# Kernel optimization log

Measured on AMD Instinct MI355X. Metric: run time of the kernel, lower is better.

The kernel has to match this reference:

```python
import jax, jax.numpy as jnp
import numpy as np

N_EMBD = 384
NUM_HEADS = 6
HEAD_SIZE = 64


def setup_inputs() -> dict:
    key = jax.random.key(0)
    k1, k2, k3, k4 = jax.random.split(key, 4)
    B, T = 32, 1024
    x = jax.random.normal(k1, (B, T, N_EMBD), dtype=jnp.float32)
    # torch Linear(n_embd, 3*n_embd, bias=False): store as [in, out]
    s_attn = 1.0 / np.sqrt(N_EMBD)
    W_attn = jax.random.uniform(k2, (N_EMBD, 3 * N_EMBD), dtype=jnp.float32, minval=-s_attn, maxval=s_attn)
    W_proj = jax.random.uniform(k3, (N_EMBD, N_EMBD), dtype=jnp.float32, minval=-s_attn, maxval=s_attn)
    b_proj = jax.random.uniform(k4, (N_EMBD,), dtype=jnp.float32, minval=-s_attn, maxval=s_attn)
    return {"x": x, "W_attn": W_attn, "W_proj": W_proj, "b_proj": b_proj}


def reference(x, W_attn, W_proj, b_proj):
    B, T, C = x.shape
    H, D = NUM_HEADS, HEAD_SIZE
    qkv = x @ W_attn                      # [B, T, 3C]
    q, k, v = jnp.split(qkv, 3, axis=2)   # each [B, T, C]
    # [B, H, T, D]
    q = q.reshape(B, T, H, D).transpose(0, 2, 1, 3)
    k = k.reshape(B, T, H, D).transpose(0, 2, 1, 3)
    v = v.reshape(B, T, H, D).transpose(0, 2, 1, 3)
    scale = 1.0 / jnp.sqrt(jnp.asarray(D, dtype=x.dtype))
    scores = jnp.einsum("bhqd,bhkd->bhqk", q, k) * scale  # [B, H, T, T]
    causal = jnp.tril(jnp.ones((T, T), dtype=bool))
    scores = jnp.where(causal, scores, jnp.asarray(-jnp.inf, dtype=scores.dtype))
    attn = jax.nn.softmax(scores, axis=-1)
    y = jnp.einsum("bhqk,bhkd->bhqd", attn, v)             # [B, H, T, D]
    y = y.transpose(0, 2, 1, 3).reshape(B, T, C)
    # dropout is inactive in eval mode
    return y @ W_proj + b_proj
```

## Files before the change

kernel.cpp:

```cpp
#include <hip/hip_runtime.h>
#include <hip/hip_bf16.h>

#define DEV __device__ __forceinline__

typedef __attribute__((ext_vector_type(4))) float f32x4;
typedef __bf16 bf16x8 __attribute__((ext_vector_type(8)));

static DEV unsigned short f2bf(float f) {
    union { float f; unsigned u; } x; x.f = f;
    unsigned r = x.u + 0x7fffu + ((x.u >> 16) & 1u);
    return (unsigned short)(r >> 16);
}

static DEV f32x4 zero4() { f32x4 v; v[0] = 0.f; v[1] = 0.f; v[2] = 0.f; v[3] = 0.f; return v; }

#define GL1(p) ((const __attribute__((address_space(1))) void*)(p))
#define LDS3(p) ((__attribute__((address_space(3))) void*)(p))


__global__ __launch_bounds__(256) void k_prep(
    const float* __restrict__ x, unsigned short* __restrict__ xb,
    const float* __restrict__ Wa, unsigned short* __restrict__ WaT,
    const float* __restrict__ Wp, unsigned short* __restrict__ WpT)
{
    int i = blockIdx.x * 256 + threadIdx.x;
    if (i < 3145728) {
        float4 v = reinterpret_cast<const float4*>(x)[i];
        ushort4 o;
        o.x = f2bf(v.x); o.y = f2bf(v.y); o.z = f2bf(v.z); o.w = f2bf(v.w);
        reinterpret_cast<ushort4*>(xb)[i] = o;
    } else if (i < 3145728 + 442368) {
        int j = i - 3145728;
        int n = j / 384, k = j - n * 384;
        WaT[j] = f2bf(Wa[(size_t)k * 1152 + n]);
    } else if (i < 3145728 + 442368 + 147456) {
        int j = i - (3145728 + 442368);
        int n = j / 384, k = j - n * 384;
        WpT[j] = f2bf(Wp[(size_t)k * 384 + n]);
    }
}


template <int SWAP>
static DEV void gemm_mainloop(
    const unsigned short* __restrict__ A,
    const unsigned short* __restrict__ B,
    int m0, int n0, int tid,
    f32x4 (&acc)[4][4],
    unsigned short (&lA)[128][64], unsigned short (&lB)[128][64])
{
    const int K = 384;
    const int w = tid >> 6, lane = tid & 63;
    const int wm = (w >> 1) * 64, wn = (w & 1) * 64;
    const int lr = lane & 15, lg = lane >> 4;
    const int lrow = lane >> 3;
    const int lcol = ((lane & 7) ^ lrow) * 8;

    for (int kb = 0; kb < K; kb += 64) {
        __syncthreads();
#pragma unroll
        for (int c = 0; c < 4; ++c) {
            int rb = (w * 4 + c) * 8;
            __builtin_amdgcn_global_load_lds(GL1(&A[(size_t)(m0 + rb + lrow) * K + kb + lcol]),
                                             LDS3(&lA[rb][0]), 16, 0, 0);
            __builtin_amdgcn_global_load_lds(GL1(&B[(size_t)(n0 + rb + lrow) * K + kb + lcol]),
                                             LDS3(&lB[rb][0]), 16, 0, 0);
        }
        __syncthreads();

        bf16x8 af[4][2], bfr[4][2];
#pragma unroll
        for (int kc = 0; kc < 2; ++kc) {
#pragma unroll
            for (int t = 0; t < 4; ++t) {
                int ga = ((kc * 4 + lg) ^ (lr & 7)) * 8;
                af[t][kc]  = *(const bf16x8*)&lA[wm + t * 16 + lr][ga];
                bfr[t][kc] = *(const bf16x8*)&lB[wn + t * 16 + lr][ga];
            }
        }
#pragma unroll
        for (int kc = 0; kc < 2; ++kc)
#pragma unroll
            for (int mt = 0; mt < 4; ++mt)
#pragma unroll
                for (int nt = 0; nt < 4; ++nt)
                    acc[mt][nt] = SWAP
                        ? __builtin_amdgcn_mfma_f32_16x16x32_bf16(bfr[nt][kc], af[mt][kc], acc[mt][nt], 0, 0, 0)
                        : __builtin_amdgcn_mfma_f32_16x16x32_bf16(af[mt][kc], bfr[nt][kc], acc[mt][nt], 0, 0, 0);
    }
}


__global__ __launch_bounds__(256) void k_gemm_qkv(
    const unsigned short* __restrict__ A,
    const unsigned short* __restrict__ B,
    unsigned short* __restrict__ Qb, unsigned short* __restrict__ Kb,
    unsigned short* __restrict__ Vb)
{
    __shared__ unsigned short lA[128][64];
    __shared__ unsigned short lB[128][64];

    const int bid = blockIdx.x;
    const int xcd = bid & 7, s = bid >> 3;
    const int mi = xcd * 32 + s / 9;
    const int cj = s % 9;
    const int m0 = mi * 128, n0 = cj * 128;

    const int tid = threadIdx.x;
    const int w = tid >> 6, lane = tid & 63;
    const int wm = (w >> 1) * 64, wn = (w & 1) * 64;
    const int lr = lane & 15, lg = lane >> 4;

    f32x4 acc[4][4];
#pragma unroll
    for (int i = 0; i < 4; i++)
#pragma unroll
        for (int j = 0; j < 4; j++) acc[i][j] = zero4();

    if (cj < 6) {
        gemm_mainloop<1>(A, B, m0, n0, tid, acc, lA, lB);
        const int which = cj / 3;
#pragma unroll
        for (int mt = 0; mt < 4; ++mt) {
            int row = m0 + wm + mt * 16 + lr;
            int bb = row >> 10, tloc = row & 1023;
#pragma unroll
            for (int nt = 0; nt < 4; ++nt) {
                int col = n0 + wn + nt * 16 + lg * 4;
                int c = col - which * 384;
                int hh = c >> 6, d0 = c & 63;
                size_t bh = (size_t)bb * 6 + hh;
                int kc = (d0 >> 5) & 1;
                int ln = (tloc & 15) + 16 * ((d0 >> 3) & 3);
                int e0 = d0 & 7;
                union { __bf16 h4[4]; uint2 u; } pk;
                if (which == 0) {
#pragma unroll
                    for (int r = 0; r < 4; ++r)
                        pk.h4[r] = (__bf16)(acc[mt][nt][r] * 0.18033688f);
                    int qt = tloc >> 5, fmt = (tloc >> 4) & 1;
                    *(uint2*)&Qb[((((bh * 32 + qt) * 2 + fmt) * 2 + kc) * 64 + ln) * 8 + e0] = pk.u;
                } else {
#pragma unroll
                    for (int r = 0; r < 4; ++r)
                        pk.h4[r] = (__bf16)acc[mt][nt][r];
                    int ktt = tloc >> 6, fnt = (tloc >> 4) & 3;
                    *(uint2*)&Kb[((((bh * 16 + ktt) * 4 + fnt) * 2 + kc) * 64 + ln) * 8 + e0] = pk.u;
                }
            }
        }
    } else {
        gemm_mainloop<0>(A, B, m0, n0, tid, acc, lA, lB);
#pragma unroll
        for (int nt = 0; nt < 4; ++nt) {
            int col = n0 + wn + nt * 16 + lr;
            int c = col - 768;
            int hh = c >> 6, d = c & 63;
            int fnt = d >> 4;
#pragma unroll
            for (int mt = 0; mt < 4; ++mt) {
                int row0 = m0 + wm + mt * 16 + lg * 4;
                int bb = row0 >> 10, t0 = row0 & 1023;
                size_t bh = (size_t)bb * 6 + hh;
                int ktt = t0 >> 6, kc = (t0 >> 5) & 1, e0 = t0 & 7;
                int ln = (d & 15) + 16 * ((t0 >> 3) & 3);
                union { __bf16 h4[4]; uint2 u; } pk;
#pragma unroll
                for (int r = 0; r < 4; ++r)
                    pk.h4[r] = (__bf16)acc[mt][nt][r];
                *(uint2*)&Vb[((((bh * 16 + ktt) * 4 + fnt) * 2 + kc) * 64 + ln) * 8 + e0] = pk.u;
            }
        }
    }
}


__global__ __launch_bounds__(256) void k_gemm_proj(
    const unsigned short* __restrict__ A,
    const unsigned short* __restrict__ B,
    const float* __restrict__ bias, float* __restrict__ Out)
{
    __shared__ unsigned short lA[128][64];
    __shared__ unsigned short lB[128][64];

    const int bid = blockIdx.x;
    const int xcd = bid & 7, s = bid >> 3;
    const int mi = xcd * 32 + s / 3;
    const int cj = s % 3;
    const int m0 = mi * 128, n0 = cj * 128;

    const int tid = threadIdx.x;
    const int w = tid >> 6, lane = tid & 63;
    const int wm = (w >> 1) * 64, wn = (w & 1) * 64;
    const int lr = lane & 15, lg = lane >> 4;

    f32x4 acc[4][4];
#pragma unroll
    for (int i = 0; i < 4; i++)
#pragma unroll
        for (int j = 0; j < 4; j++) acc[i][j] = zero4();

    gemm_mainloop<1>(A, B, m0, n0, tid, acc, lA, lB);

#pragma unroll
    for (int mt = 0; mt < 4; ++mt) {
        int row = m0 + wm + mt * 16 + lr;
#pragma unroll
        for (int nt = 0; nt < 4; ++nt) {
            int col = n0 + wn + nt * 16 + lg * 4;
            f32x4 bv = *(const f32x4*)&bias[col];
            f32x4 ov;
#pragma unroll
            for (int r = 0; r < 4; ++r) ov[r] = acc[mt][nt][r] + bv[r];
            *(f32x4*)&Out[(size_t)row * 384 + col] = ov;
        }
    }
}


template <int NTM, bool MASK>
static DEV void attn_tile(
    const unsigned short* lKt, const unsigned short* lVt, unsigned short* lPw,
    const bf16x8 (&qf)[2][2], f32x4 (&o)[2][4], float (&ls)[2],
    int kt, int qw, int lane)
{
    constexpr int KCM = NTM / 2;
    const int lr = lane & 15, lg = lane >> 4;

    bf16x8 kf[NTM][2];
#pragma unroll
    for (int nt = 0; nt < NTM; ++nt)
#pragma unroll
        for (int kc = 0; kc < 2; ++kc)
            kf[nt][kc] = *(const bf16x8*)&lKt[(nt * 2 + kc) * 512 + lane * 8];

    bf16x8 vf[4][KCM];
#pragma unroll
    for (int nt = 0; nt < 4; ++nt)
#pragma unroll
        for (int kc = 0; kc < KCM; ++kc)
            vf[nt][kc] = *(const bf16x8*)&lVt[(nt * 2 + kc) * 512 + lane * 8];

    f32x4 st[2][NTM];
#pragma unroll
    for (int mt = 0; mt < 2; ++mt)
#pragma unroll
        for (int nt = 0; nt < NTM; ++nt) st[mt][nt] = zero4();

    __builtin_amdgcn_s_setprio(1);
#pragma unroll
    for (int kc = 0; kc < 2; ++kc)
#pragma unroll
        for (int mt = 0; mt < 2; ++mt)
#pragma unroll
            for (int nt = 0; nt < NTM; ++nt)
                st[mt][nt] = __builtin_amdgcn_mfma_f32_16x16x32_bf16(kf[nt][kc], qf[mt][kc], st[mt][nt], 0, 0, 0);
    __builtin_amdgcn_s_setprio(0);

#pragma unroll
    for (int mt = 0; mt < 2; ++mt) {
#pragma unroll
        for (int nt = 0; nt < NTM; ++nt) {
            union { __bf16 hh[4]; uint2 u; } pk;
            float e[4];
#pragma unroll
            for (int r = 0; r < 4; ++r) {
                float ev = __builtin_amdgcn_exp2f(st[mt][nt][r]);
                if (MASK) {
                    int kg = kt * 64 + nt * 16 + lg * 4 + r;
                    int qg = qw + mt * 16 + lr;
                    if (kg > qg) ev = 0.f;
                }
                e[r] = ev;
                pk.hh[r] = (__bf16)ev;
            }
            ls[mt] += (e[0] + e[1]) + (e[2] + e[3]);
            int ln2 = lr + 16 * ((nt & 1) * 2 + (lg >> 1));
            *(uint2*)&lPw[(mt * 2 + (nt >> 1)) * 512 + ln2 * 8 + (lg & 1) * 4] = pk.u;
        }
    }

    bf16x8 pf[2][KCM];
#pragma unroll
    for (int mt = 0; mt < 2; ++mt)
#pragma unroll
        for (int kc = 0; kc < KCM; ++kc)
            pf[mt][kc] = *(const bf16x8*)&lPw[(mt * 2 + kc) * 512 + lane * 8];

    __builtin_amdgcn_s_setprio(1);
#pragma unroll
    for (int mt = 0; mt < 2; ++mt)
#pragma unroll
        for (int nt = 0; nt < 4; ++nt)
#pragma unroll
            for (int kc = 0; kc < KCM; ++kc)
                o[mt][nt] = __builtin_amdgcn_mfma_f32_16x16x32_bf16(vf[nt][kc], pf[mt][kc], o[mt][nt], 0, 0, 0);
    __builtin_amdgcn_s_setprio(0);
}

static DEV void attn_pass(
    int gg, int w, int lane, int b, int h, int bh,
    const unsigned short* __restrict__ Qf,
    const unsigned short* __restrict__ Kbh,
    const unsigned short* __restrict__ Vbh,
    unsigned short* __restrict__ Y,
    unsigned short (&lK)[2][4096], unsigned short (&lV)[2][4096],
    unsigned short* lPw)
{
    const int lr = lane & 15, lg = lane >> 4;
    const int qt = 4 * gg + w;
    const int qw = qt * 32;
    const int nkt = qt / 2 + 1;
    const int nsteps = 2 * gg + 2;

    bf16x8 qf[2][2];
#pragma unroll
    for (int mt = 0; mt < 2; ++mt)
#pragma unroll
        for (int kc = 0; kc < 2; ++kc)
            qf[mt][kc] = *(const bf16x8*)&Qf[((((size_t)bh * 32 + qt) * 2 + mt) * 2 + kc) * 512 + lane * 8];

    f32x4 o[2][4];
    float ls[2] = {0.f, 0.f};
#pragma unroll
    for (int mt = 0; mt < 2; ++mt)
#pragma unroll
        for (int nt = 0; nt < 4; ++nt) o[mt][nt] = zero4();

    __syncthreads();

#pragma unroll
    for (int i = 0; i < 2; ++i) {
        __builtin_amdgcn_global_load_lds(GL1(Kbh + (size_t)w * 1024 + i * 512 + lane * 8),
                                         LDS3(&lK[0][w * 1024 + i * 512]), 16, 0, 0);
        __builtin_amdgcn_global_load_lds(GL1(Vbh + (size_t)w * 1024 + i * 512 + lane * 8),
                                         LDS3(&lV[0][w * 1024 + i * 512]), 16, 0, 0);
    }

    for (int kt = 0; kt < nsteps; ++kt) {
        __syncthreads();
        if (kt + 1 < nsteps) {
            int nb = (kt + 1) & 1;
#pragma unroll
            for (int i = 0; i < 2; ++i) {
                __builtin_amdgcn_global_load_lds(GL1(Kbh + (size_t)(kt + 1) * 4096 + w * 1024 + i * 512 + lane * 8),
                                                 LDS3(&lK[nb][w * 1024 + i * 512]), 16, 0, 0);
                __builtin_amdgcn_global_load_lds(GL1(Vbh + (size_t)(kt + 1) * 4096 + w * 1024 + i * 512 + lane * 8),
                                                 LDS3(&lV[nb][w * 1024 + i * 512]), 16, 0, 0);
            }
        }
        if (kt < nkt) {
            const unsigned short* lKt = lK[kt & 1];
            const unsigned short* lVt = lV[kt & 1];
            if (kt == nkt - 1) {
                if (qt & 1) attn_tile<4, true>(lKt, lVt, lPw, qf, o, ls, kt, qw, lane);
                else        attn_tile<2, true>(lKt, lVt, lPw, qf, o, ls, kt, qw, lane);
            } else {
                attn_tile<4, false>(lKt, lVt, lPw, qf, o, ls, kt, qw, lane);
            }
        }
    }

    float inv[2];
#pragma unroll
    for (int mt = 0; mt < 2; ++mt) {
        float s = ls[mt];
        s += __shfl_xor(s, 16);
        s += __shfl_xor(s, 32);
        inv[mt] = 1.0f / s;
    }
#pragma unroll
    for (int mt = 0; mt < 2; ++mt) {
#pragma unroll
        for (int nt = 0; nt < 4; ++nt) {
            union { __bf16 h4[4]; uint2 u; } pk;
#pragma unroll
            for (int r = 0; r < 4; ++r) pk.h4[r] = (__bf16)(o[mt][nt][r] * inv[mt]);
            *(uint2*)&Y[((size_t)b * 1024 + qw + mt * 16 + lr) * 384 + h * 64 + nt * 16 + lg * 4] = pk.u;
        }
    }
}

__global__ __launch_bounds__(256, 3) void k_attn(
    const unsigned short* __restrict__ Qf,
    const unsigned short* __restrict__ Kf,
    const unsigned short* __restrict__ Vf,
    unsigned short* __restrict__ Y)
{
    __shared__ unsigned short lK[2][4096];
    __shared__ unsigned short lV[2][4096];
    __shared__ unsigned short lPf[4][2048];

    const int tid = threadIdx.x;
    const int w = tid >> 6, lane = tid & 63;
    const int bh = blockIdx.x;
    const int g = blockIdx.y;
    const int b = bh / 6, h = bh - b * 6;

    const unsigned short* Kbh = Kf + (size_t)bh * 65536;
    const unsigned short* Vbh = Vf + (size_t)bh * 65536;

    attn_pass(g,     w, lane, b, h, bh, Qf, Kbh, Vbh, Y, lK, lV, lPf[w]);
    attn_pass(7 - g, w, lane, b, h, bh, Qf, Kbh, Vbh, Y, lK, lV, lPf[w]);
}


extern "C" void kernel_launch(void* const* d_in, const int* in_sizes, int n_in,
                              void* d_out, int out_size, void* d_ws, size_t ws_size,
                              hipStream_t stream)
{
    const float* x  = (const float*)d_in[0];
    const float* Wa = (const float*)d_in[1];
    const float* Wp = (const float*)d_in[2];
    const float* bp = (const float*)d_in[3];
    float* out = (float*)d_out;

    char* ws = (char*)d_ws;
    unsigned short* xb  = (unsigned short*)(ws);
    unsigned short* WaT = (unsigned short*)(ws + 25165824);
    unsigned short* WpT = (unsigned short*)(ws + 26050560);
    unsigned short* Qb  = (unsigned short*)(ws + 26345472);
    unsigned short* Kb  = (unsigned short*)(ws + 51511296);
    unsigned short* Vtb = (unsigned short*)(ws + 76677120);

    k_prep<<<14592, 256, 0, stream>>>(x, xb, Wa, WaT, Wp, WpT);
    k_gemm_qkv<<<2304, 256, 0, stream>>>(xb, WaT, Qb, Kb, Vtb);
    k_attn<<<dim3(192, 4), 256, 0, stream>>>(Qb, Kb, Vtb, xb);
    k_gemm_proj<<<768, 256, 0, stream>>>(xb, WpT, bp, out);
}
```

Measured before the change: 122.8 us.

## Process two adjacent query tiles per wave, sharing K/V register fragments

Restructures the attention kernel so each wave owns two consecutive 32-row query tiles (A and B). K and V fragments are loaded from LDS once per key tile and reused by both query tiles, which halves LDS read traffic per MFMA. The two balanced passes per block are replaced by a single pass, with block scheduling reversed so the heaviest groups launch first. Occupancy is lowered from 3 to 2 blocks per SM in launch_bounds to make room for the extra accumulator and Q registers, which reduces latency hiding and may leave load imbalance across blocks.

```diff
diff --git a/kernel.cpp b/kernel.cpp
--- a/kernel.cpp
+++ b/kernel.cpp
@@ -219,27 +219,12 @@
 
 
 template <int NTM, bool MASK>
-static DEV void attn_tile(
-    const unsigned short* lKt, const unsigned short* lVt, unsigned short* lPw,
+static DEV void attn_qtile(
+    const bf16x8 (&kf)[4][2], const bf16x8 (&vf)[4][2],
     const bf16x8 (&qf)[2][2], f32x4 (&o)[2][4], float (&ls)[2],
-    int kt, int qw, int lane)
+    unsigned short* lPw, int kt, int qw, int lr, int lg)
 {
     constexpr int KCM = NTM / 2;
-    const int lr = lane & 15, lg = lane >> 4;
-
-    bf16x8 kf[NTM][2];
-#pragma unroll
-    for (int nt = 0; nt < NTM; ++nt)
-#pragma unroll
-        for (int kc = 0; kc < 2; ++kc)
-            kf[nt][kc] = *(const bf16x8*)&lKt[(nt * 2 + kc) * 512 + lane * 8];
-
-    bf16x8 vf[4][KCM];
-#pragma unroll
-    for (int nt = 0; nt < 4; ++nt)
-#pragma unroll
-        for (int kc = 0; kc < KCM; ++kc)
-            vf[nt][kc] = *(const bf16x8*)&lVt[(nt * 2 + kc) * 512 + lane * 8];
 
     f32x4 st[2][NTM];
 #pragma unroll
@@ -285,7 +270,7 @@
     for (int mt = 0; mt < 2; ++mt)
 #pragma unroll
         for (int kc = 0; kc < KCM; ++kc)
-            pf[mt][kc] = *(const bf16x8*)&lPw[(mt * 2 + kc) * 512 + lane * 8];
+            pf[mt][kc] = *(const bf16x8*)&lPw[(mt * 2 + kc) * 512 + (lr + 16 * lg) * 8];
 
     __builtin_amdgcn_s_setprio(1);
 #pragma unroll
@@ -298,36 +283,70 @@
     __builtin_amdgcn_s_setprio(0);
 }
 
-static DEV void attn_pass(
-    int gg, int w, int lane, int b, int h, int bh,
+static DEV void attn_out(const f32x4 (&o)[2][4], const float (&ls)[2],
+                         int qw, int b, int h, int lr, int lg,
+                         unsigned short* __restrict__ Y)
+{
+    float inv[2];
+#pragma unroll
+    for (int mt = 0; mt < 2; ++mt) {
+        float s = ls[mt];
+        s += __shfl_xor(s, 16);
+        s += __shfl_xor(s, 32);
+        inv[mt] = 1.0f / s;
+    }
+#pragma unroll
+    for (int mt = 0; mt < 2; ++mt) {
+#pragma unroll
+        for (int nt = 0; nt < 4; ++nt) {
+            union { __bf16 h4[4]; uint2 u; } pk;
+#pragma unroll
+            for (int r = 0; r < 4; ++r) pk.h4[r] = (__bf16)(o[mt][nt][r] * inv[mt]);
+            *(uint2*)&Y[((size_t)b * 1024 + qw + mt * 16 + lr) * 384 + h * 64 + nt * 16 + lg * 4] = pk.u;
+        }
+    }
+}
+
+__global__ __launch_bounds__(256, 2) void k_attn(
     const unsigned short* __restrict__ Qf,
-    const unsigned short* __restrict__ Kbh,
-    const unsigned short* __restrict__ Vbh,
-    unsigned short* __restrict__ Y,
-    unsigned short (&lK)[2][4096], unsigned short (&lV)[2][4096],
-    unsigned short* lPw)
-{
+    const unsigned short* __restrict__ Kf,
+    const unsigned short* __restrict__ Vf,
+    unsigned short* __restrict__ Y)
+{
+    __shared__ unsigned short lK[2][4096];
+    __shared__ unsigned short lV[2][4096];
+    __shared__ unsigned short lPf[4][2048];
+
+    const int tid = threadIdx.x;
+    const int w = tid >> 6, lane = tid & 63;
     const int lr = lane & 15, lg = lane >> 4;
-    const int qt = 4 * gg + w;
-    const int qw = qt * 32;
-    const int nkt = qt / 2 + 1;
-    const int nsteps = 2 * gg + 2;
-
-    bf16x8 qf[2][2];
+    const int bh = blockIdx.x;
+    const int pg = 3 - blockIdx.y;
+    const int p = 4 * pg + w;
+    const int qtA = 2 * p, qtB = 2 * p + 1;
+    const int qwA = qtA * 32, qwB = qtB * 32;
+    const int nkt = p + 1;
+    const int nsteps = 4 * pg + 4;
+    const int b = bh / 6, h = bh - b * 6;
+
+    const unsigned short* Kbh = Kf + (size_t)bh * 65536;
+    const unsigned short* Vbh = Vf + (size_t)bh * 65536;
+
+    bf16x8 qfA[2][2], qfB[2][2];
 #pragma unroll
     for (int mt = 0; mt < 2; ++mt)
 #pragma unroll
-        for (int kc = 0; kc < 2; ++kc)
-            qf[mt][kc] = *(const bf16x8*)&Qf[((((size_t)bh * 32 + qt) * 2 + mt) * 2 + kc) * 512 + lane * 8];
-
-    f32x4 o[2][4];
-    float ls[2] = {0.f, 0.f};
+        for (int kc = 0; kc < 2; ++kc) {
+            qfA[mt][kc] = *(const bf16x8*)&Qf[((((size_t)bh * 32 + qtA) * 2 + mt) * 2 + kc) * 512 + lane * 8];
+            qfB[mt][kc] = *(const bf16x8*)&Qf[((((size_t)bh * 32 + qtB) * 2 + mt) * 2 + kc) * 512 + lane * 8];
+        }
+
+    f32x4 oA[2][4], oB[2][4];
+    float lsA[2] = {0.f, 0.f}, lsB[2] = {0.f, 0.f};
 #pragma unroll
     for (int mt = 0; mt < 2; ++mt)
 #pragma unroll
-        for (int nt = 0; nt < 4; ++nt) o[mt][nt] = zero4();
-
-    __syncthreads();
+        for (int nt = 0; nt < 4; ++nt) { oA[mt][nt] = zero4(); oB[mt][nt] = zero4(); }
 
 #pragma unroll
     for (int i = 0; i < 2; ++i) {
@@ -352,56 +371,28 @@
         if (kt < nkt) {
             const unsigned short* lKt = lK[kt & 1];
             const unsigned short* lVt = lV[kt & 1];
+
+            bf16x8 kf[4][2], vf[4][2];
+#pragma unroll
+            for (int nt = 0; nt < 4; ++nt)
+#pragma unroll
+                for (int kc = 0; kc < 2; ++kc) {
+                    kf[nt][kc] = *(const bf16x8*)&lKt[(nt * 2 + kc) * 512 + lane * 8];
+                    vf[nt][kc] = *(const bf16x8*)&lVt[(nt * 2 + kc) * 512 + lane * 8];
+                }
+
             if (kt == nkt - 1) {
-                if (qt & 1) attn_tile<4, true>(lKt, lVt, lPw, qf, o, ls, kt, qw, lane);
-                else        attn_tile<2, true>(lKt, lVt, lPw, qf, o, ls, kt, qw, lane);
+                attn_qtile<2, true>(kf, vf, qfA, oA, lsA, lPf[w], kt, qwA, lr, lg);
+                attn_qtile<4, true>(kf, vf, qfB, oB, lsB, lPf[w], kt, qwB, lr, lg);
             } else {
-                attn_tile<4, false>(lKt, lVt, lPw, qf, o, ls, kt, qw, lane);
-            }
-        }
-    }
-
-    float inv[2];
-#pragma unroll
-    for (int mt = 0; mt < 2; ++mt) {
-        float s = ls[mt];
-        s += __shfl_xor(s, 16);
-        s += __shfl_xor(s, 32);
-        inv[mt] = 1.0f / s;
-    }
-#pragma unroll
-    for (int mt = 0; mt < 2; ++mt) {
-#pragma unroll
-        for (int nt = 0; nt < 4; ++nt) {
-            union { __bf16 h4[4]; uint2 u; } pk;
-#pragma unroll
-            for (int r = 0; r < 4; ++r) pk.h4[r] = (__bf16)(o[mt][nt][r] * inv[mt]);
-            *(uint2*)&Y[((size_t)b * 1024 + qw + mt * 16 + lr) * 384 + h * 64 + nt * 16 + lg * 4] = pk.u;
-        }
-    }
-}
-
-__global__ __launch_bounds__(256, 3) void k_attn(
-    const unsigned short* __restrict__ Qf,
-    const unsigned short* __restrict__ Kf,
-    const unsigned short* __restrict__ Vf,
-    unsigned short* __restrict__ Y)
-{
-    __shared__ unsigned short lK[2][4096];
-    __shared__ unsigned short lV[2][4096];
-    __shared__ unsigned short lPf[4][2048];
-
-    const int tid = threadIdx.x;
-    const int w = tid >> 6, lane = tid & 63;
-    const int bh = blockIdx.x;
-    const int g = blockIdx.y;
-    const int b = bh / 6, h = bh - b * 6;
-
-    const unsigned short* Kbh = Kf + (size_t)bh * 65536;
-    const unsigned short* Vbh = Vf + (size_t)bh * 65536;
-
-    attn_pass(g,     w, lane, b, h, bh, Qf, Kbh, Vbh, Y, lK, lV, lPf[w]);
-    attn_pass(7 - g, w, lane, b, h, bh, Qf, Kbh, Vbh, Y, lK, lV, lPf[w]);
+                attn_qtile<4, false>(kf, vf, qfA, oA, lsA, lPf[w], kt, qwA, lr, lg);
+                attn_qtile<4, false>(kf, vf, qfB, oB, lsB, lPf[w], kt, qwB, lr, lg);
+            }
+        }
+    }
+
+    attn_out(oA, lsA, qwA, b, h, lr, lg, Y);
+    attn_out(oB, lsB, qwB, b, h, lr, lg, Y);
 }
 
 
```

New measurement: 126.8 us. 1.03x slower.
